# Kernel optimization log

Hardware: AMD Instinct MI355X
Metric: run time of the kernel (lower is better)

Reference implementation:

```python
import jax, jax.numpy as jnp
import numpy as np

N = 30000      # nodes of type 'A'
IN = 128       # in_channels = hidden*2
H = 64         # hidden_channels
OUT = 64
M = 4          # number of metapaths (seq len for attention)
E = 480000     # edges per relation
NH = 8         # num_heads
HD = OUT // NH # head dim = 8
FF = 2048      # transformer dim_feedforward (torch default)
L = 2          # transformer layers
EPS = 1e-5


def setup_inputs() -> dict:
    key = jax.random.key(0)
    ks = iter(jax.random.split(key, 64))
    nk = lambda: next(ks)
    rn = lambda shape, s=0.05: (jax.random.normal(nk(), shape, jnp.float32) * s)
    x = jax.random.normal(nk(), (N, IN), jnp.float32)
    edge_index = jax.random.randint(nk(), (M, 2, E), 0, N, dtype=jnp.int32)
    counts = jnp.array([3.0, 1.0, 2.0, 2.0], jnp.float32)
    mp_weights = counts / counts.sum()
    inp = dict(x=x, edge_index=edge_index, mp_weights=mp_weights,
               W0=rn((M, H, IN)), b0=rn((M, H)), Wl=rn((M, H, IN)), bl=rn((M, H)),
               W1=rn((M, H, IN)), b1=rn((M, H)), Wo=rn((M, OUT, H)), bo=rn((M, OUT)),
               tinw=rn((L, 3 * OUT, OUT)), tinb=rn((L, 3 * OUT)),
               tow=rn((L, OUT, OUT)), tob=rn((L, OUT)),
               ln1g=jnp.ones((L, OUT)), ln1b=jnp.zeros((L, OUT)),
               ff1w=rn((L, FF, OUT)), ff1b=rn((L, FF)),
               ff2w=rn((L, OUT, FF)), ff2b=rn((L, OUT)),
               ln2g=jnp.ones((L, OUT)), ln2b=jnp.zeros((L, OUT)),
               r1w=rn((OUT, OUT)), r1b=rn((OUT,)), r2w=rn((1, OUT)), r2b=rn((1,)))
    return inp


def _layer_norm(v, g, b):
    mu = v.mean(-1, keepdims=True)
    var = ((v - mu) ** 2).mean(-1, keepdims=True)
    return (v - mu) / jnp.sqrt(var + EPS) * g + b


def reference(x, edge_index, mp_weights, W0, b0, Wl, bl, W1, b1, Wo, bo,
              tinw, tinb, tow, tob, ln1g, ln1b, ff1w, ff1b, ff2w, ff2b,
              ln2g, ln2b, r1w, r1b, r2w, r2b):
    n = x.shape[0]
    # ---- per-metapath GNN: gather + scatter-add + 3 fused linears ----
    embs = []
    for m in range(M):
        src, dst = edge_index[m, 0], edge_index[m, 1]
        # flow='target_to_source', aggr='add': agg[i] = sum_{e: src[e]==i} h[dst[e]]
        agg = jnp.zeros_like(x).at[src].add(x[dst])
        # w_l(agg) + w_0(h) + w_1(x), with h == x (forward passes x=h=h_dict[dst])
        h = jax.nn.relu(agg @ Wl[m].T + bl[m] + x @ (W0[m] + W1[m]).T + (b0[m] + b1[m]))
        embs.append(h @ Wo[m].T + bo[m])  # out_proj on updated start-type feats
    e = jnp.stack(embs, axis=1) * mp_weights[None, :, None]  # (N, M, OUT)

    # ---- 2-layer post-norm TransformerEncoder (batch_first, eval/no dropout) ----
    for l in range(L):
        qkv = e @ tinw[l].T + tinb[l]                       # (N, M, 3*OUT)
        q, k, v = jnp.split(qkv, 3, axis=-1)
        split = lambda t: t.reshape(n, M, NH, HD).transpose(0, 2, 1, 3)  # (N,NH,M,HD)
        q, k, v = split(q), split(k), split(v)
        attn = jax.nn.softmax(jnp.einsum('nhqd,nhkd->nhqk', q, k) / np.float32(np.sqrt(HD)), axis=-1)
        o = jnp.einsum('nhqk,nhkd->nhqd', attn, v).transpose(0, 2, 1, 3).reshape(n, M, OUT)
        o = o @ tow[l].T + tob[l]
        e = _layer_norm(e + o, ln1g[l], ln1b[l])
        f = jax.nn.relu(e @ ff1w[l].T + ff1b[l]) @ ff2w[l].T + ff2b[l]
        e = _layer_norm(e + f, ln2g[l], ln2b[l])

    pooled = e.mean(axis=1)                                  # (N, OUT)
    out = jax.nn.relu(pooled @ r1w.T + r1b) @ r2w.T + r2b    # (N, 1)
    return out[:, 0]
```

## Files before the change

kernel.cpp:

```cpp
#include <hip/hip_runtime.h>
#include <hip/hip_bf16.h>
#include <math.h>

#define N_NODES 30000
#define M_P     4
#define E_EDGES 480000
#define N_TOK   (N_NODES * 4)
#define N_ROWS  (M_P * N_NODES)
#define SLOTS   30
#define LN_EPS  1e-5f

typedef short bf16x8 __attribute__((ext_vector_type(8)));
typedef float f32x4  __attribute__((ext_vector_type(4)));
#define MFMA_B16(a, b, c) __builtin_amdgcn_mfma_f32_16x16x32_bf16(a, b, c, 0, 0, 0)

__device__ inline unsigned short f2bf(float f) {
    union { float f; unsigned u; } v; v.f = f;
    unsigned r = v.u + 0x7fffu + ((v.u >> 16) & 1u);
    return (unsigned short)(r >> 16);
}
__device__ inline unsigned pack2bf(float a, float b) {
    union { __hip_bfloat162 h; unsigned u; } cv;
    cv.h = __float22bfloat162_rn(make_float2(a, b));
    return cv.u;
}
__device__ inline float bf2f(short s) {
    union { unsigned u; float f; } v; v.u = ((unsigned)(unsigned short)s) << 16;
    return v.f;
}
__device__ inline bf16x8 mk_frag(const float4& a, const float4& b) {
    union { uint4 u; bf16x8 v; } cv;
    cv.u = make_uint4(pack2bf(a.x, a.y), pack2bf(a.z, a.w),
                      pack2bf(b.x, b.y), pack2bf(b.z, b.w));
    return cv.v;
}

__global__ __launch_bounds__(256) void k_wshuf_gnn(
    const float* __restrict__ Wl, const float* __restrict__ W0, const float* __restrict__ W1,
    unsigned short* __restrict__ wgnn)
{
    const int g = blockIdx.x * 256 + threadIdx.x;
    const int which = g >> 15;
    const int r = g & 32767;
    const int m = r >> 13;
    const int r2 = r & 8191;
    const int row = r2 >> 7, k = r2 & 127;
    const int ot = row >> 4, mm = row & 15;
    const int hh = k >> 5, q = (k >> 3) & 3, j = k & 7;
    float v;
    if (which == 0) v = Wl[(m * 64 + row) * 128 + k];
    else            v = W0[(m * 64 + row) * 128 + k] + W1[(m * 64 + row) * 128 + k];
    wgnn[((which * 4 + m) * 16 + ot * 4 + hh) * 512 + (q * 16 + mm) * 8 + j] = f2bf(v);
}

__global__ __launch_bounds__(256) void k_lin_mfma(
    const float* __restrict__ x, const unsigned short* __restrict__ wgnn,
    const float* __restrict__ b0, const float* __restrict__ bl, const float* __restrict__ b1,
    float* __restrict__ y, float* __restrict__ z)
{
    const int t = threadIdx.x;
    const int w = t >> 6, lane = t & 63;
    const int m_ = lane & 15, qc = lane >> 4;
    const int mw = blockIdx.y;
    const int which = mw >> 2, m = mw & 3;
    const int node = blockIdx.x * 64 + w * 16 + m_;

    bf16x8 xb[4];
    #pragma unroll
    for (int hh = 0; hh < 4; ++hh) {
        float4 a = make_float4(0.f, 0.f, 0.f, 0.f), b = a;
        if (node < N_NODES) {
            a = *(const float4*)(x + node * 128 + hh * 32 + qc * 8);
            b = *(const float4*)(x + node * 128 + hh * 32 + qc * 8 + 4);
        }
        xb[hh] = mk_frag(a, b);
    }

    const unsigned short* Wg = wgnn + mw * 16 * 512;
    f32x4 acc[4];
    #pragma unroll
    for (int ot = 0; ot < 4; ++ot) {
        f32x4 c = {};
        if (which) {
            const int o = m * 64 + ot * 16 + qc * 4;
            const float4 v0 = *(const float4*)(b0 + o);
            const float4 v1 = *(const float4*)(b1 + o);
            const float4 vl = *(const float4*)(bl + o);
            c[0] = v0.x + v1.x + vl.x; c[1] = v0.y + v1.y + vl.y;
            c[2] = v0.z + v1.z + vl.z; c[3] = v0.w + v1.w + vl.w;
        }
        #pragma unroll
        for (int hh = 0; hh < 4; ++hh) {
            const bf16x8 wa = *(const bf16x8*)(Wg + (ot * 4 + hh) * 512 + lane * 8);
            c = MFMA_B16(wa, xb[hh], c);
        }
        acc[ot] = c;
    }
    float* outp = which ? z : y;
    if (node < N_NODES) {
        #pragma unroll
        for (int ot = 0; ot < 4; ++ot)
            *(float4*)(outp + ((size_t)m * N_NODES + node) * 64 + ot * 16 + qc * 4) =
                *(float4*)&acc[ot];
    }
}

__global__ __launch_bounds__(256) void k_fill(
    const int* __restrict__ ei, unsigned short* __restrict__ bins,
    const float* __restrict__ y, float* __restrict__ aggh)
{
    const int base = blockIdx.x * 1024 + threadIdx.x;
    int rows[4], dsts[4];
    #pragma unroll
    for (int i = 0; i < 4; ++i) {
        const int g = base + i * 256;
        const int m = g / E_EDGES;
        const int e = g - m * E_EDGES;
        rows[i] = m * N_NODES + ei[(m * 2) * E_EDGES + e];
        dsts[i] = ei[(m * 2 + 1) * E_EDGES + e];
    }
    int pos[4];
    #pragma unroll
    for (int i = 0; i < 4; ++i)
        pos[i] = atomicAdd((int*)bins + rows[i] * 16, 1);
    #pragma unroll
    for (int i = 0; i < 4; ++i) {
        if (pos[i] < SLOTS) {
            bins[rows[i] * 32 + 2 + pos[i]] = (unsigned short)dsts[i];
        } else {
            const int m = rows[i] / N_NODES;
            const float* yr = y + ((size_t)m * N_NODES + dsts[i]) * 64;
            for (int f = 0; f < 64; ++f)
                unsafeAtomicAdd(&aggh[(size_t)rows[i] * 64 + f], yr[f]);
        }
    }
}

__global__ __launch_bounds__(256) void k_gather(
    const unsigned short* __restrict__ bins,
    const float* __restrict__ y, float* __restrict__ aggh)
{
    const int w = threadIdx.x >> 6, lane = threadIdx.x & 63;
    const int row = blockIdx.x * 4 + w;
    const int m = row / N_NODES;
    const float* ym = y + (size_t)m * N_NODES * 64;
    const int v = (lane < 32) ? bins[row * 32 + lane] : 0;
    const int v0 = __shfl(v, 0), v1 = __shfl(v, 1);
    const int tot = (v0 & 0xffff) | (v1 << 16);
    const int cnt = min(tot, SLOTS);
    float a0 = (tot > SLOTS) ? aggh[(size_t)row * 64 + lane] : 0.f;
    float a1 = 0.f, a2 = 0.f, a3 = 0.f;
    int j = 0;
    for (; j + 4 <= cnt; j += 4) {
        const int r0 = __shfl(v, j + 2), r1 = __shfl(v, j + 3);
        const int r2 = __shfl(v, j + 4), r3 = __shfl(v, j + 5);
        a0 += ym[r0 * 64 + lane]; a1 += ym[r1 * 64 + lane];
        a2 += ym[r2 * 64 + lane]; a3 += ym[r3 * 64 + lane];
    }
    for (; j < cnt; ++j) {
        const int r = __shfl(v, j + 2);
        a0 += ym[r * 64 + lane];
    }
    aggh[(size_t)row * 64 + lane] = (a0 + a1) + (a2 + a3);
}

__global__ __launch_bounds__(256) void k_emb(
    const float* __restrict__ aggh, const float* __restrict__ z,
    const float* __restrict__ Wo, const float* __restrict__ bo,
    const float* __restrict__ mpw, float* __restrict__ e)
{
    __shared__ float hT[64][20];
    __shared__ float WoT[64][64];
    const int t = threadIdx.x;
    const int node0 = blockIdx.x * 16;

    for (int m = 0; m < 4; ++m) {
        #pragma unroll
        for (int i = 0; i < 4; ++i) {
            const int o  = (t & 15) + 16 * i;
            const int kq = t >> 4;
            const float4 v = *(const float4*)(Wo + (m * 64 + o) * 64 + kq * 4);
            WoT[kq * 4 + 0][o] = v.x; WoT[kq * 4 + 1][o] = v.y;
            WoT[kq * 4 + 2][o] = v.z; WoT[kq * 4 + 3][o] = v.w;
        }
        {
            const int node = t & 15, kq = t >> 4;
            const int n = node0 + node;
            const float4 a = *(const float4*)(aggh + (m * N_NODES + n) * 64 + kq * 4);
            const float4 b = *(const float4*)(z + (m * N_NODES + n) * 64 + kq * 4);
            hT[kq * 4 + 0][node] = fmaxf(a.x + b.x, 0.f);
            hT[kq * 4 + 1][node] = fmaxf(a.y + b.y, 0.f);
            hT[kq * 4 + 2][node] = fmaxf(a.z + b.z, 0.f);
            hT[kq * 4 + 3][node] = fmaxf(a.w + b.w, 0.f);
        }
        __syncthreads();
        const int o = t & 63, nl4 = (t >> 6) * 4;
        float acc[4] = {};
        #pragma unroll 8
        for (int k = 0; k < 64; ++k) {
            const float bw = WoT[k][o];
            const float4 a = *(const float4*)&hT[k][nl4];
            acc[0] += a.x * bw; acc[1] += a.y * bw; acc[2] += a.z * bw; acc[3] += a.w * bw;
        }
        const float bb = bo[m * 64 + o];
        const float w  = mpw[m];
        #pragma unroll
        for (int i = 0; i < 4; ++i)
            e[((node0 + nl4 + i) * 4 + m) * 64 + o] = (acc[i] + bb) * w;
        __syncthreads();
    }
}

__global__ __launch_bounds__(256, 3) void k_attn_mfma(
    const float* __restrict__ e,
    const unsigned short* __restrict__ wqkv_s, const float* __restrict__ tinb,
    const unsigned short* __restrict__ tow_s, const float* __restrict__ tob,
    const float* __restrict__ ln1g, const float* __restrict__ ln1b,
    float* __restrict__ eout, int l)
{
    __shared__ __align__(16) short QK[17408];
    __shared__ __align__(16) short Vb[9216];
    const int t = threadIdx.x;
    const int w = t >> 6, lane = t & 63;
    const int m_ = lane & 15, qc = lane >> 4;
    const int tok0 = blockIdx.x * 128;
    short* QKw = &QK[w * 4352];
    short* Vw  = &Vb[w * 2304];

    bf16x8 xb[2][2];
    #pragma unroll
    for (int nt = 0; nt < 2; ++nt)
        #pragma unroll
        for (int h = 0; h < 2; ++h) {
            const int tok = tok0 + w * 32 + nt * 16 + m_;
            const int k0 = h * 32 + qc * 8;
            float4 a = make_float4(0.f, 0.f, 0.f, 0.f), b = a;
            if (tok < N_TOK) {
                a = *(const float4*)(e + tok * 64 + k0);
                b = *(const float4*)(e + tok * 64 + k0 + 4);
            }
            xb[nt][h] = mk_frag(a, b);
        }

    const unsigned short* Wq = wqkv_s + l * 12288;
    f32x4 acc[12][2];
    #pragma unroll
    for (int ft = 0; ft < 12; ++ft) {
        const bf16x8 wa0 = *(const bf16x8*)(Wq + (ft * 2 + 0) * 512 + lane * 8);
        const bf16x8 wa1 = *(const bf16x8*)(Wq + (ft * 2 + 1) * 512 + lane * 8);
        const float4 bv = *(const float4*)(tinb + l * 192 + ft * 16 + qc * 4);
        f32x4 c0; c0[0] = bv.x; c0[1] = bv.y; c0[2] = bv.z; c0[3] = bv.w;
        f32x4 c1 = c0;
        c0 = MFMA_B16(wa0, xb[0][0], c0); c0 = MFMA_B16(wa1, xb[0][1], c0);
        c1 = MFMA_B16(wa0, xb[1][0], c1); c1 = MFMA_B16(wa1, xb[1][1], c1);
        acc[ft][0] = c0; acc[ft][1] = c1;
    }
    #pragma unroll
    for (int ft = 0; ft < 8; ++ft)
        #pragma unroll
        for (int nt = 0; nt < 2; ++nt) {
            const int addr = (nt * 16 + m_) * 136 + ft * 16 + qc * 4;
            *(uint2*)&QKw[addr] = make_uint2(pack2bf(acc[ft][nt][0], acc[ft][nt][1]),
                                             pack2bf(acc[ft][nt][2], acc[ft][nt][3]));
        }
    #pragma unroll
    for (int ft = 8; ft < 12; ++ft)
        #pragma unroll
        for (int nt = 0; nt < 2; ++nt) {
            const int addr = (nt * 16 + m_) * 72 + (ft - 8) * 16 + qc * 4;
            *(uint2*)&Vw[addr] = make_uint2(pack2bf(acc[ft][nt][0], acc[ft][nt][1]),
                                            pack2bf(acc[ft][nt][2], acc[ft][nt][3]));
        }

    {
        const int node = lane >> 3, head = lane & 7;
        float kk[4][8], vv[4][8], qv[4][8];
        #pragma unroll
        for (int j2 = 0; j2 < 4; ++j2) {
            const bf16x8 kr = *(const bf16x8*)&QKw[(node * 4 + j2) * 136 + 64 + head * 8];
            const bf16x8 vr = *(const bf16x8*)&Vw[(node * 4 + j2) * 72 + head * 8];
            const bf16x8 qr = *(const bf16x8*)&QKw[(node * 4 + j2) * 136 + head * 8];
            #pragma unroll
            for (int d = 0; d < 8; ++d) {
                kk[j2][d] = bf2f(kr[d]); vv[j2][d] = bf2f(vr[d]); qv[j2][d] = bf2f(qr[d]);
            }
        }
        const float scale = 0.35355339059327373f;
        const int nt2 = node >> 2, hq = head >> 2, qq = head & 3;
        #pragma unroll
        for (int i = 0; i < 4; ++i) {
            float s[4];
            #pragma unroll
            for (int j2 = 0; j2 < 4; ++j2) {
                float a2 = 0.f;
                #pragma unroll
                for (int d = 0; d < 8; ++d) a2 += qv[i][d] * kk[j2][d];
                s[j2] = a2 * scale;
            }
            const float mx = fmaxf(fmaxf(s[0], s[1]), fmaxf(s[2], s[3]));
            float p[4], sum = 0.f;
            #pragma unroll
            for (int j2 = 0; j2 < 4; ++j2) { p[j2] = __expf(s[j2] - mx); sum += p[j2]; }
            const float inv = 1.f / sum;
            float o[8];
            #pragma unroll
            for (int d = 0; d < 8; ++d)
                o[d] = (p[0] * vv[0][d] + p[1] * vv[1][d] + p[2] * vv[2][d] + p[3] * vv[3][d]) * inv;
            const int n = (node & 3) * 4 + i;
            *(uint4*)&QKw[(nt2 * 2 + hq) * 512 + qq * 128 + n * 8] =
                make_uint4(pack2bf(o[0], o[1]), pack2bf(o[2], o[3]),
                           pack2bf(o[4], o[5]), pack2bf(o[6], o[7]));
        }
    }

    bf16x8 ob[2][2];
    #pragma unroll
    for (int nt = 0; nt < 2; ++nt)
        #pragma unroll
        for (int h = 0; h < 2; ++h)
            ob[nt][h] = *(const bf16x8*)&QKw[(nt * 2 + h) * 512 + lane * 8];
    const unsigned short* Tw = tow_s + l * 4096;
    f32x4 acc2[4][2] = {};
    #pragma unroll
    for (int ot = 0; ot < 4; ++ot) {
        const bf16x8 t0 = *(const bf16x8*)(Tw + (ot * 2 + 0) * 512 + lane * 8);
        const bf16x8 t1 = *(const bf16x8*)(Tw + (ot * 2 + 1) * 512 + lane * 8);
        acc2[ot][0] = MFMA_B16(t0, ob[0][0], acc2[ot][0]);
        acc2[ot][0] = MFMA_B16(t1, ob[0][1], acc2[ot][0]);
        acc2[ot][1] = MFMA_B16(t0, ob[1][0], acc2[ot][1]);
        acc2[ot][1] = MFMA_B16(t1, ob[1][1], acc2[ot][1]);
    }

    float4 tbv[4], gv[4], bv2[4];
    #pragma unroll
    for (int ot = 0; ot < 4; ++ot) {
        const int o = l * 64 + ot * 16 + qc * 4;
        tbv[ot] = *(const float4*)(tob + o);
        gv[ot]  = *(const float4*)(ln1g + o);
        bv2[ot] = *(const float4*)(ln1b + o);
    }
    #pragma unroll
    for (int nt = 0; nt < 2; ++nt) {
        const int tok = tok0 + w * 32 + nt * 16 + m_;
        const bool valid = tok < N_TOK;
        float v[4][4];
        float s = 0.f;
        #pragma unroll
        for (int ot = 0; ot < 4; ++ot) {
            float4 rs = make_float4(0.f, 0.f, 0.f, 0.f);
            if (valid) rs = *(const float4*)(e + tok * 64 + ot * 16 + qc * 4);
            v[ot][0] = acc2[ot][nt][0] + tbv[ot].x + rs.x;
            v[ot][1] = acc2[ot][nt][1] + tbv[ot].y + rs.y;
            v[ot][2] = acc2[ot][nt][2] + tbv[ot].z + rs.z;
            v[ot][3] = acc2[ot][nt][3] + tbv[ot].w + rs.w;
            s += v[ot][0] + v[ot][1] + v[ot][2] + v[ot][3];
        }
        s += __shfl_xor(s, 16); s += __shfl_xor(s, 32);
        const float mean = s * (1.f / 64.f);
        float vs = 0.f;
        #pragma unroll
        for (int ot = 0; ot < 4; ++ot)
            #pragma unroll
            for (int r = 0; r < 4; ++r) { v[ot][r] -= mean; vs += v[ot][r] * v[ot][r]; }
        vs += __shfl_xor(vs, 16); vs += __shfl_xor(vs, 32);
        const float rr = rsqrtf(vs * (1.f / 64.f) + LN_EPS);
        if (valid) {
            #pragma unroll
            for (int ot = 0; ot < 4; ++ot) {
                float4 o4 = make_float4(v[ot][0] * rr * gv[ot].x + bv2[ot].x,
                                        v[ot][1] * rr * gv[ot].y + bv2[ot].y,
                                        v[ot][2] * rr * gv[ot].z + bv2[ot].z,
                                        v[ot][3] * rr * gv[ot].w + bv2[ot].w);
                *(float4*)(eout + tok * 64 + ot * 16 + qc * 4) = o4;
            }
        }
    }
}

__global__ __launch_bounds__(256) void k_wshuf(
    const float* __restrict__ ff1w, const float* __restrict__ ff2w,
    const float* __restrict__ tinw, const float* __restrict__ tow,
    unsigned short* __restrict__ w1s, unsigned short* __restrict__ w2s,
    unsigned short* __restrict__ wqkv_s, unsigned short* __restrict__ tow_s)
{
    const int g = blockIdx.x * 256 + threadIdx.x;
    {
        const int l = g >> 17, r2 = g & 131071;
        const int f = r2 >> 6, k = r2 & 63;
        const int c = f >> 6, fc = f & 63, ft = fc >> 4, m = fc & 15;
        const int h = k >> 5, q = (k >> 3) & 3, j = k & 7;
        w1s[l * 131072 + c * 4096 + (ft * 2 + h) * 512 + (q * 16 + m) * 8 + j] = f2bf(ff1w[g]);
    }
    {
        const int l = g >> 17, r2 = g & 131071;
        const int o = r2 >> 11, f = r2 & 2047;
        const int c = f >> 6, fc = f & 63, h = fc >> 5, q = (fc >> 3) & 3, j = fc & 7;
        const int ot = o >> 4, m = o & 15;
        w2s[l * 131072 + c * 4096 + (ot * 2 + h) * 512 + (q * 16 + m) * 8 + j] = f2bf(ff2w[g]);
    }
    if (g < 2 * 192 * 64) {
        const int l = g / 12288, r2 = g - l * 12288;
        const int f = r2 >> 6, k = r2 & 63;
        const int ft = f >> 4, m = f & 15;
        const int h = k >> 5, q = (k >> 3) & 3, j = k & 7;
        wqkv_s[l * 12288 + (ft * 2 + h) * 512 + (q * 16 + m) * 8 + j] = f2bf(tinw[g]);
    }
    if (g < 2 * 64 * 64) {
        const int l = g >> 12, r2 = g & 4095;
        const int o = r2 >> 6, k = r2 & 63;
        const int ot = o >> 4, m = o & 15;
        const int h = k >> 5, q = (k >> 3) & 3, j = k & 7;
        tow_s[l * 4096 + (ot * 2 + h) * 512 + (q * 16 + m) * 8 + j] = f2bf(tow[g]);
    }
}

__global__ __launch_bounds__(256, 4) void k_ffn_mfma(
    const float* __restrict__ e,
    const unsigned short* __restrict__ w1s, const unsigned short* __restrict__ w2s,
    const float* __restrict__ ff1b, const float* __restrict__ ff2b,
    const float* __restrict__ ln2g, const float* __restrict__ ln2b,
    float* __restrict__ eout, int l)
{
    __shared__ __align__(16) short Act[8192];
    __shared__ __align__(16) short Wb[8192];
    const int t = threadIdx.x;
    const int w = t >> 6, lane = t & 63;
    const int m_ = lane & 15, qc = lane >> 4;
    const int tok0 = blockIdx.x * 128;
    short* Aw = &Act[w * 2048];

    bf16x8 xb[2][2];
    #pragma unroll
    for (int nt = 0; nt < 2; ++nt)
        #pragma unroll
        for (int h = 0; h < 2; ++h) {
            const int tok = tok0 + w * 32 + nt * 16 + m_;
            const int k0 = h * 32 + qc * 8;
            float4 a = make_float4(0.f, 0.f, 0.f, 0.f), b = a;
            if (tok < N_TOK) {
                a = *(const float4*)(e + tok * 64 + k0);
                b = *(const float4*)(e + tok * 64 + k0 + 4);
            }
            xb[nt][h] = mk_frag(a, b);
        }

    const uint4* gw1 = (const uint4*)(w1s + l * 131072);
    const uint4* gw2 = (const uint4*)(w2s + l * 131072);
    uint4 p0 = gw1[t], p1 = gw1[t + 256], p2 = gw2[t], p3 = gw2[t + 256];
    *(uint4*)&Wb[t * 8] = p0;            *(uint4*)&Wb[(t + 256) * 8] = p1;
    *(uint4*)&Wb[4096 + t * 8] = p2;     *(uint4*)&Wb[4096 + (t + 256) * 8] = p3;

    f32x4 acc[4][2] = {};

    for (int c = 0; c < 32; ++c) {
        __syncthreads();
        if (c < 31) {
            p0 = gw1[(c + 1) * 512 + t];       p1 = gw1[(c + 1) * 512 + t + 256];
            p2 = gw2[(c + 1) * 512 + t];       p3 = gw2[(c + 1) * 512 + t + 256];
        }
        #pragma unroll
        for (int ft = 0; ft < 4; ++ft) {
            const bf16x8 wa0 = *(const bf16x8*)&Wb[(ft * 2 + 0) * 512 + lane * 8];
            const bf16x8 wa1 = *(const bf16x8*)&Wb[(ft * 2 + 1) * 512 + lane * 8];
            const float4 bv = *(const float4*)(ff1b + l * 2048 + c * 64 + ft * 16 + qc * 4);
            f32x4 c0; c0[0] = bv.x; c0[1] = bv.y; c0[2] = bv.z; c0[3] = bv.w;
            f32x4 c1 = c0;
            c0 = MFMA_B16(wa0, xb[0][0], c0); c0 = MFMA_B16(wa1, xb[0][1], c0);
            c1 = MFMA_B16(wa0, xb[1][0], c1); c1 = MFMA_B16(wa1, xb[1][1], c1);
            const int ha = ft >> 1, qa = (ft & 1) * 2 + (qc >> 1), jo = (qc & 1) * 4;
            const int boff = ha * 512 + qa * 128 + m_ * 8 + jo;
            *(uint2*)&Aw[boff] =
                make_uint2(pack2bf(fmaxf(c0[0], 0.f), fmaxf(c0[1], 0.f)),
                           pack2bf(fmaxf(c0[2], 0.f), fmaxf(c0[3], 0.f)));
            *(uint2*)&Aw[boff + 1024] =
                make_uint2(pack2bf(fmaxf(c1[0], 0.f), fmaxf(c1[1], 0.f)),
                           pack2bf(fmaxf(c1[2], 0.f), fmaxf(c1[3], 0.f)));
        }
        bf16x8 ab[2][2];
        #pragma unroll
        for (int nt = 0; nt < 2; ++nt)
            #pragma unroll
            for (int h = 0; h < 2; ++h)
                ab[nt][h] = *(const bf16x8*)&Aw[(nt * 2 + h) * 512 + lane * 8];
        #pragma unroll
        for (int ot = 0; ot < 4; ++ot) {
            const bf16x8 w20 = *(const bf16x8*)&Wb[4096 + (ot * 2 + 0) * 512 + lane * 8];
            const bf16x8 w21 = *(const bf16x8*)&Wb[4096 + (ot * 2 + 1) * 512 + lane * 8];
            acc[ot][0] = MFMA_B16(w20, ab[0][0], acc[ot][0]);
            acc[ot][0] = MFMA_B16(w21, ab[0][1], acc[ot][0]);
            acc[ot][1] = MFMA_B16(w20, ab[1][0], acc[ot][1]);
            acc[ot][1] = MFMA_B16(w21, ab[1][1], acc[ot][1]);
        }
        __syncthreads();
        if (c < 31) {
            *(uint4*)&Wb[t * 8] = p0;            *(uint4*)&Wb[(t + 256) * 8] = p1;
            *(uint4*)&Wb[4096 + t * 8] = p2;     *(uint4*)&Wb[4096 + (t + 256) * 8] = p3;
        }
    }

    float4 fb2v[4], gv[4], bv2[4];
    #pragma unroll
    for (int ot = 0; ot < 4; ++ot) {
        const int o = l * 64 + ot * 16 + qc * 4;
        fb2v[ot] = *(const float4*)(ff2b + o);
        gv[ot]   = *(const float4*)(ln2g + o);
        bv2[ot]  = *(const float4*)(ln2b + o);
    }
    #pragma unroll
    for (int nt = 0; nt < 2; ++nt) {
        const int tok = tok0 + w * 32 + nt * 16 + m_;
        const bool valid = tok < N_TOK;
        float v[4][4];
        float s = 0.f;
        #pragma unroll
        for (int ot = 0; ot < 4; ++ot) {
            float4 rs = make_float4(0.f, 0.f, 0.f, 0.f);
            if (valid) rs = *(const float4*)(e + tok * 64 + ot * 16 + qc * 4);
            v[ot][0] = acc[ot][nt][0] + fb2v[ot].x + rs.x;
            v[ot][1] = acc[ot][nt][1] + fb2v[ot].y + rs.y;
            v[ot][2] = acc[ot][nt][2] + fb2v[ot].z + rs.z;
            v[ot][3] = acc[ot][nt][3] + fb2v[ot].w + rs.w;
            s += v[ot][0] + v[ot][1] + v[ot][2] + v[ot][3];
        }
        s += __shfl_xor(s, 16); s += __shfl_xor(s, 32);
        const float mean = s * (1.f / 64.f);
        float vs = 0.f;
        #pragma unroll
        for (int ot = 0; ot < 4; ++ot)
            #pragma unroll
            for (int r = 0; r < 4; ++r) { v[ot][r] -= mean; vs += v[ot][r] * v[ot][r]; }
        vs += __shfl_xor(vs, 16); vs += __shfl_xor(vs, 32);
        const float rr = rsqrtf(vs * (1.f / 64.f) + LN_EPS);
        if (valid) {
            #pragma unroll
            for (int ot = 0; ot < 4; ++ot) {
                float4 o4 = make_float4(v[ot][0] * rr * gv[ot].x + bv2[ot].x,
                                        v[ot][1] * rr * gv[ot].y + bv2[ot].y,
                                        v[ot][2] * rr * gv[ot].z + bv2[ot].z,
                                        v[ot][3] * rr * gv[ot].w + bv2[ot].w);
                *(float4*)(eout + tok * 64 + ot * 16 + qc * 4) = o4;
            }
        }
    }
}

__global__ __launch_bounds__(256) void k_reg(
    const float* __restrict__ e,
    const float* __restrict__ r1w, const float* __restrict__ r1b,
    const float* __restrict__ r2w, const float* __restrict__ r2b,
    float* __restrict__ out)
{
    __shared__ float r1T[64][64];
    __shared__ float pld[4][64];
    const int t = threadIdx.x;
    #pragma unroll
    for (int i = 0; i < 4; ++i) {
        const int j  = (t & 15) + 16 * i;
        const int kq = t >> 4;
        const float4 v = *(const float4*)(r1w + j * 64 + kq * 4);
        r1T[kq * 4 + 0][j] = v.x; r1T[kq * 4 + 1][j] = v.y;
        r1T[kq * 4 + 2][j] = v.z; r1T[kq * 4 + 3][j] = v.w;
    }
    const int w = t >> 6, lane = t & 63;
    const int n = blockIdx.x * 4 + w;
    const float p = 0.25f * (e[(n * 4 + 0) * 64 + lane] + e[(n * 4 + 1) * 64 + lane] +
                             e[(n * 4 + 2) * 64 + lane] + e[(n * 4 + 3) * 64 + lane]);
    pld[w][lane] = p;
    __syncthreads();
    float acc = r1b[lane];
    #pragma unroll 8
    for (int k = 0; k < 64; ++k) acc += pld[w][k] * r1T[k][lane];
    acc = fmaxf(acc, 0.f);
    float partial = acc * r2w[lane];
    partial += __shfl_xor(partial, 1);  partial += __shfl_xor(partial, 2);
    partial += __shfl_xor(partial, 4);  partial += __shfl_xor(partial, 8);
    partial += __shfl_xor(partial, 16); partial += __shfl_xor(partial, 32);
    if (lane == 0) out[n] = partial + r2b[0];
}

extern "C" void kernel_launch(void* const* d_in, const int* in_sizes, int n_in,
                              void* d_out, int out_size, void* d_ws, size_t ws_size,
                              hipStream_t stream) {
    const float* x    = (const float*)d_in[0];
    const int*   ei   = (const int*)d_in[1];
    const float* mpw  = (const float*)d_in[2];
    const float* W0   = (const float*)d_in[3];
    const float* b0   = (const float*)d_in[4];
    const float* Wl   = (const float*)d_in[5];
    const float* bl   = (const float*)d_in[6];
    const float* W1   = (const float*)d_in[7];
    const float* b1   = (const float*)d_in[8];
    const float* Wo   = (const float*)d_in[9];
    const float* bo   = (const float*)d_in[10];
    const float* tinw = (const float*)d_in[11];
    const float* tinb = (const float*)d_in[12];
    const float* tow  = (const float*)d_in[13];
    const float* tob  = (const float*)d_in[14];
    const float* ln1g = (const float*)d_in[15];
    const float* ln1b = (const float*)d_in[16];
    const float* ff1w = (const float*)d_in[17];
    const float* ff1b = (const float*)d_in[18];
    const float* ff2w = (const float*)d_in[19];
    const float* ff2b = (const float*)d_in[20];
    const float* ln2g = (const float*)d_in[21];
    const float* ln2b = (const float*)d_in[22];
    const float* r1w  = (const float*)d_in[23];
    const float* r1b  = (const float*)d_in[24];
    const float* r2w  = (const float*)d_in[25];
    const float* r2b  = (const float*)d_in[26];

    const size_t CH = (size_t)M_P * N_NODES * 64;
    float* y    = (float*)d_ws;
    float* zz   = y + CH;
    float* aggh = zz + CH;
    float* e    = aggh + CH;
    unsigned short* w1s    = (unsigned short*)y;
    unsigned short* w2s    = w1s + 262144;
    unsigned short* wqkv_s = w2s + 262144;
    unsigned short* tow_s  = wqkv_s + 24576;
    unsigned short* bins = (unsigned short*)e;
    unsigned short* wgnn = (unsigned short*)((char*)e + 8 * 1024 * 1024);

    hipMemsetAsync(bins, 0, (size_t)N_ROWS * 64, stream);
    hipMemsetAsync(aggh, 0, CH * sizeof(float), stream);
    k_wshuf_gnn<<<256, 256, 0, stream>>>(Wl, W0, W1, wgnn);
    k_lin_mfma<<<dim3(469, 8), 256, 0, stream>>>(x, wgnn, b0, bl, b1, y, zz);
    k_fill<<<(M_P * E_EDGES) / 1024, 256, 0, stream>>>(ei, bins, y, aggh);
    k_gather<<<N_ROWS / 4, 256, 0, stream>>>(bins, y, aggh);
    k_emb<<<N_NODES / 16, 256, 0, stream>>>(aggh, zz, Wo, bo, mpw, e);
    k_wshuf<<<1024, 256, 0, stream>>>(ff1w, ff2w, tinw, tow, w1s, w2s, wqkv_s, tow_s);
    for (int l = 0; l < 2; ++l) {
        k_attn_mfma<<<(N_TOK + 127) / 128, 256, 0, stream>>>(e, wqkv_s, tinb, tow_s, tob,
                                                             ln1g, ln1b, e, l);
        k_ffn_mfma<<<(N_TOK + 127) / 128, 256, 0, stream>>>(e, w1s, w2s, ff1b, ff2b,
                                                            ln2g, ln2b, e, l);
    }
    k_reg<<<N_NODES / 4, 256, 0, stream>>>(e, r1w, r1b, r2w, r2b, (float*)d_out);
}
```

Before: 596.6 us.

## Fuse edge binning with GNN linear and weight shuffles; add overflow edge list

Edge binning and the per-metapath MFMA linear now run as one launch using disjoint block ranges. This is possible because binning no longer needs y: edges beyond the slot capacity go to a global overflow list instead of doing immediate float atomics into aggh. Each linear block now converts and shuffles its GNN weight tile into LDS itself. The transformer weight shuffle moves into extra blocks of the embedding kernel, and the 30 MB aggh memset is gone. The aim is to cut launches, memsets and serialisation between stages. The cost is redundant per-block weight conversion and a linear scan of the overflow list for every overflowing row, with a fixed capacity that silently drops entries beyond 65536.

```diff
diff --git a/kernel.cpp b/kernel.cpp
--- a/kernel.cpp
+++ b/kernel.cpp
@@ -8,7 +8,11 @@
 #define N_TOK   (N_NODES * 4)
 #define N_ROWS  (M_P * N_NODES)
 #define SLOTS   30
+#define OVF_CAP 65536
 #define LN_EPS  1e-5f
+
+#define NB_FILL 1875
+#define NB_LIN  3752
 
 typedef short bf16x8 __attribute__((ext_vector_type(8)));
 typedef float f32x4  __attribute__((ext_vector_type(4)));
@@ -35,109 +39,109 @@
     return cv.v;
 }
 
-__global__ __launch_bounds__(256) void k_wshuf_gnn(
+__global__ __launch_bounds__(256) void k_phaseA(
+    const int* __restrict__ ei, unsigned short* __restrict__ bins,
+    int* __restrict__ ovf_cnt, int2* __restrict__ ovf,
+    const float* __restrict__ x,
     const float* __restrict__ Wl, const float* __restrict__ W0, const float* __restrict__ W1,
-    unsigned short* __restrict__ wgnn)
-{
-    const int g = blockIdx.x * 256 + threadIdx.x;
-    const int which = g >> 15;
-    const int r = g & 32767;
-    const int m = r >> 13;
-    const int r2 = r & 8191;
-    const int row = r2 >> 7, k = r2 & 127;
-    const int ot = row >> 4, mm = row & 15;
-    const int hh = k >> 5, q = (k >> 3) & 3, j = k & 7;
-    float v;
-    if (which == 0) v = Wl[(m * 64 + row) * 128 + k];
-    else            v = W0[(m * 64 + row) * 128 + k] + W1[(m * 64 + row) * 128 + k];
-    wgnn[((which * 4 + m) * 16 + ot * 4 + hh) * 512 + (q * 16 + mm) * 8 + j] = f2bf(v);
-}
-
-__global__ __launch_bounds__(256) void k_lin_mfma(
-    const float* __restrict__ x, const unsigned short* __restrict__ wgnn,
     const float* __restrict__ b0, const float* __restrict__ bl, const float* __restrict__ b1,
     float* __restrict__ y, float* __restrict__ z)
 {
+    __shared__ __align__(16) short Wf[8192];
+    const int bid = blockIdx.x;
     const int t = threadIdx.x;
-    const int w = t >> 6, lane = t & 63;
-    const int m_ = lane & 15, qc = lane >> 4;
-    const int mw = blockIdx.y;
-    const int which = mw >> 2, m = mw & 3;
-    const int node = blockIdx.x * 64 + w * 16 + m_;
-
-    bf16x8 xb[4];
-    #pragma unroll
-    for (int hh = 0; hh < 4; ++hh) {
-        float4 a = make_float4(0.f, 0.f, 0.f, 0.f), b = a;
+
+    if (bid < NB_FILL) {
+        const int base = bid * 1024 + t;
+        int rows[4], dsts[4];
+        #pragma unroll
+        for (int i = 0; i < 4; ++i) {
+            const int g = base + i * 256;
+            const int m = g / E_EDGES;
+            const int e = g - m * E_EDGES;
+            rows[i] = m * N_NODES + ei[(m * 2) * E_EDGES + e];
+            dsts[i] = ei[(m * 2 + 1) * E_EDGES + e];
+        }
+        int pos[4];
+        #pragma unroll
+        for (int i = 0; i < 4; ++i)
+            pos[i] = atomicAdd((int*)bins + rows[i] * 16, 1);
+        #pragma unroll
+        for (int i = 0; i < 4; ++i) {
+            if (pos[i] < SLOTS) {
+                bins[rows[i] * 32 + 2 + pos[i]] = (unsigned short)dsts[i];
+            } else {
+                const int ix = atomicAdd(ovf_cnt, 1);
+                if (ix < OVF_CAP) ovf[ix] = make_int2(rows[i], dsts[i]);
+            }
+        }
+    } else {
+        const int lid = bid - NB_FILL;
+        const int bx = lid % 469;
+        const int by = lid / 469;
+        const int which = by >> 2, m = by & 3;
+        const int w = t >> 6, lane = t & 63;
+        const int m_ = lane & 15, qc = lane >> 4;
+        const int node = bx * 64 + w * 16 + m_;
+
+        #pragma unroll
+        for (int i = 0; i < 32; ++i) {
+            const int d = t + 256 * i;
+            const int fg = d >> 9, rem = d & 511;
+            const int qmm = rem >> 3, j = d & 7;
+            const int q = qmm >> 4, mm = qmm & 15;
+            const int ot = fg >> 2, hh = fg & 3;
+            const int row = ot * 16 + mm, k = hh * 32 + q * 8 + j;
+            float v;
+            if (which == 0) v = Wl[(m * 64 + row) * 128 + k];
+            else            v = W0[(m * 64 + row) * 128 + k] + W1[(m * 64 + row) * 128 + k];
+            Wf[d] = (short)f2bf(v);
+        }
+
+        bf16x8 xb[4];
+        #pragma unroll
+        for (int hh = 0; hh < 4; ++hh) {
+            float4 a = make_float4(0.f, 0.f, 0.f, 0.f), b = a;
+            if (node < N_NODES) {
+                a = *(const float4*)(x + node * 128 + hh * 32 + qc * 8);
+                b = *(const float4*)(x + node * 128 + hh * 32 + qc * 8 + 4);
+            }
+            xb[hh] = mk_frag(a, b);
+        }
+        __syncthreads();
+
+        f32x4 acc[4];
+        #pragma unroll
+        for (int ot = 0; ot < 4; ++ot) {
+            f32x4 c = {};
+            if (which) {
+                const int o = m * 64 + ot * 16 + qc * 4;
+                const float4 v0 = *(const float4*)(b0 + o);
+                const float4 v1 = *(const float4*)(b1 + o);
+                const float4 vl = *(const float4*)(bl + o);
+                c[0] = v0.x + v1.x + vl.x; c[1] = v0.y + v1.y + vl.y;
+                c[2] = v0.z + v1.z + vl.z; c[3] = v0.w + v1.w + vl.w;
+            }
+            #pragma unroll
+            for (int hh = 0; hh < 4; ++hh) {
+                const bf16x8 wa = *(const bf16x8*)&Wf[(ot * 4 + hh) * 512 + lane * 8];
+                c = MFMA_B16(wa, xb[hh], c);
+            }
+            acc[ot] = c;
+        }
+        float* outp = which ? z : y;
         if (node < N_NODES) {
-            a = *(const float4*)(x + node * 128 + hh * 32 + qc * 8);
-            b = *(const float4*)(x + node * 128 + hh * 32 + qc * 8 + 4);
-        }
-        xb[hh] = mk_frag(a, b);
-    }
-
-    const unsigned short* Wg = wgnn + mw * 16 * 512;
-    f32x4 acc[4];
-    #pragma unroll
-    for (int ot = 0; ot < 4; ++ot) {
-        f32x4 c = {};
-        if (which) {
-            const int o = m * 64 + ot * 16 + qc * 4;
-            const float4 v0 = *(const float4*)(b0 + o);
-            const float4 v1 = *(const float4*)(b1 + o);
-            const float4 vl = *(const float4*)(bl + o);
-            c[0] = v0.x + v1.x + vl.x; c[1] = v0.y + v1.y + vl.y;
-            c[2] = v0.z + v1.z + vl.z; c[3] = v0.w + v1.w + vl.w;
-        }
-        #pragma unroll
-        for (int hh = 0; hh < 4; ++hh) {
-            const bf16x8 wa = *(const bf16x8*)(Wg + (ot * 4 + hh) * 512 + lane * 8);
-            c = MFMA_B16(wa, xb[hh], c);
-        }
-        acc[ot] = c;
-    }
-    float* outp = which ? z : y;
-    if (node < N_NODES) {
-        #pragma unroll
-        for (int ot = 0; ot < 4; ++ot)
-            *(float4*)(outp + ((size_t)m * N_NODES + node) * 64 + ot * 16 + qc * 4) =
-                *(float4*)&acc[ot];
-    }
-}
-
-__global__ __launch_bounds__(256) void k_fill(
-    const int* __restrict__ ei, unsigned short* __restrict__ bins,
-    const float* __restrict__ y, float* __restrict__ aggh)
-{
-    const int base = blockIdx.x * 1024 + threadIdx.x;
-    int rows[4], dsts[4];
-    #pragma unroll
-    for (int i = 0; i < 4; ++i) {
-        const int g = base + i * 256;
-        const int m = g / E_EDGES;
-        const int e = g - m * E_EDGES;
-        rows[i] = m * N_NODES + ei[(m * 2) * E_EDGES + e];
-        dsts[i] = ei[(m * 2 + 1) * E_EDGES + e];
-    }
-    int pos[4];
-    #pragma unroll
-    for (int i = 0; i < 4; ++i)
-        pos[i] = atomicAdd((int*)bins + rows[i] * 16, 1);
-    #pragma unroll
-    for (int i = 0; i < 4; ++i) {
-        if (pos[i] < SLOTS) {
-            bins[rows[i] * 32 + 2 + pos[i]] = (unsigned short)dsts[i];
-        } else {
-            const int m = rows[i] / N_NODES;
-            const float* yr = y + ((size_t)m * N_NODES + dsts[i]) * 64;
-            for (int f = 0; f < 64; ++f)
-                unsafeAtomicAdd(&aggh[(size_t)rows[i] * 64 + f], yr[f]);
+            #pragma unroll
+            for (int ot = 0; ot < 4; ++ot)
+                *(float4*)(outp + ((size_t)m * N_NODES + node) * 64 + ot * 16 + qc * 4) =
+                    *(float4*)&acc[ot];
         }
     }
 }
 
 __global__ __launch_bounds__(256) void k_gather(
     const unsigned short* __restrict__ bins,
+    const int* __restrict__ ovf_cnt, const int2* __restrict__ ovf,
     const float* __restrict__ y, float* __restrict__ aggh)
 {
     const int w = threadIdx.x >> 6, lane = threadIdx.x & 63;
@@ -148,8 +152,7 @@
     const int v0 = __shfl(v, 0), v1 = __shfl(v, 1);
     const int tot = (v0 & 0xffff) | (v1 << 16);
     const int cnt = min(tot, SLOTS);
-    float a0 = (tot > SLOTS) ? aggh[(size_t)row * 64 + lane] : 0.f;
-    float a1 = 0.f, a2 = 0.f, a3 = 0.f;
+    float a0 = 0.f, a1 = 0.f, a2 = 0.f, a3 = 0.f;
     int j = 0;
     for (; j + 4 <= cnt; j += 4) {
         const int r0 = __shfl(v, j + 2), r1 = __shfl(v, j + 3);
@@ -161,19 +164,64 @@
         const int r = __shfl(v, j + 2);
         a0 += ym[r * 64 + lane];
     }
+    if (tot > SLOTS) {
+        const int no = min(*ovf_cnt, OVF_CAP);
+        for (int i2 = 0; i2 < no; ++i2) {
+            const int2 ent = ovf[i2];
+            if (ent.x == row) a0 += ym[ent.y * 64 + lane];
+        }
+    }
     aggh[(size_t)row * 64 + lane] = (a0 + a1) + (a2 + a3);
 }
 
-__global__ __launch_bounds__(256) void k_emb(
+__global__ __launch_bounds__(256) void k_emb_ws(
     const float* __restrict__ aggh, const float* __restrict__ z,
     const float* __restrict__ Wo, const float* __restrict__ bo,
-    const float* __restrict__ mpw, float* __restrict__ e)
+    const float* __restrict__ mpw, float* __restrict__ e,
+    const float* __restrict__ ff1w, const float* __restrict__ ff2w,
+    const float* __restrict__ tinw, const float* __restrict__ tow,
+    unsigned short* __restrict__ w1s, unsigned short* __restrict__ w2s,
+    unsigned short* __restrict__ wqkv_s, unsigned short* __restrict__ tow_s)
 {
     __shared__ float hT[64][20];
     __shared__ float WoT[64][64];
     const int t = threadIdx.x;
-    const int node0 = blockIdx.x * 16;
-
+    const int bid = blockIdx.x;
+
+    if (bid >= N_NODES / 16) {
+        const int g = (bid - N_NODES / 16) * 256 + t;
+        {
+            const int l = g >> 17, r2 = g & 131071;
+            const int f = r2 >> 6, k = r2 & 63;
+            const int c = f >> 6, fc = f & 63, ft = fc >> 4, m = fc & 15;
+            const int h = k >> 5, q = (k >> 3) & 3, j = k & 7;
+            w1s[l * 131072 + c * 4096 + (ft * 2 + h) * 512 + (q * 16 + m) * 8 + j] = f2bf(ff1w[g]);
+        }
+        {
+            const int l = g >> 17, r2 = g & 131071;
+            const int o = r2 >> 11, f = r2 & 2047;
+            const int c = f >> 6, fc = f & 63, h = fc >> 5, q = (fc >> 3) & 3, j = fc & 7;
+            const int ot = o >> 4, m = o & 15;
+            w2s[l * 131072 + c * 4096 + (ot * 2 + h) * 512 + (q * 16 + m) * 8 + j] = f2bf(ff2w[g]);
+        }
+        if (g < 2 * 192 * 64) {
+            const int l = g / 12288, r2 = g - l * 12288;
+            const int f = r2 >> 6, k = r2 & 63;
+            const int ft = f >> 4, m = f & 15;
+            const int h = k >> 5, q = (k >> 3) & 3, j = k & 7;
+            wqkv_s[l * 12288 + (ft * 2 + h) * 512 + (q * 16 + m) * 8 + j] = f2bf(tinw[g]);
+        }
+        if (g < 2 * 64 * 64) {
+            const int l = g >> 12, r2 = g & 4095;
+            const int o = r2 >> 6, k = r2 & 63;
+            const int ot = o >> 4, m = o & 15;
+            const int h = k >> 5, q = (k >> 3) & 3, j = k & 7;
+            tow_s[l * 4096 + (ot * 2 + h) * 512 + (q * 16 + m) * 8 + j] = f2bf(tow[g]);
+        }
+        return;
+    }
+
+    const int node0 = bid * 16;
     for (int m = 0; m < 4; ++m) {
         #pragma unroll
         for (int i = 0; i < 4; ++i) {
@@ -374,43 +422,6 @@
                 *(float4*)(eout + tok * 64 + ot * 16 + qc * 4) = o4;
             }
         }
-    }
-}
-
-__global__ __launch_bounds__(256) void k_wshuf(
-    const float* __restrict__ ff1w, const float* __restrict__ ff2w,
-    const float* __restrict__ tinw, const float* __restrict__ tow,
-    unsigned short* __restrict__ w1s, unsigned short* __restrict__ w2s,
-    unsigned short* __restrict__ wqkv_s, unsigned short* __restrict__ tow_s)
-{
-    const int g = blockIdx.x * 256 + threadIdx.x;
-    {
-        const int l = g >> 17, r2 = g & 131071;
-        const int f = r2 >> 6, k = r2 & 63;
-        const int c = f >> 6, fc = f & 63, ft = fc >> 4, m = fc & 15;
-        const int h = k >> 5, q = (k >> 3) & 3, j = k & 7;
-        w1s[l * 131072 + c * 4096 + (ft * 2 + h) * 512 + (q * 16 + m) * 8 + j] = f2bf(ff1w[g]);
-    }
-    {
-        const int l = g >> 17, r2 = g & 131071;
-        const int o = r2 >> 11, f = r2 & 2047;
-        const int c = f >> 6, fc = f & 63, h = fc >> 5, q = (fc >> 3) & 3, j = fc & 7;
-        const int ot = o >> 4, m = o & 15;
-        w2s[l * 131072 + c * 4096 + (ot * 2 + h) * 512 + (q * 16 + m) * 8 + j] = f2bf(ff2w[g]);
-    }
-    if (g < 2 * 192 * 64) {
-        const int l = g / 12288, r2 = g - l * 12288;
-        const int f = r2 >> 6, k = r2 & 63;
-        const int ft = f >> 4, m = f & 15;
-        const int h = k >> 5, q = (k >> 3) & 3, j = k & 7;
-        wqkv_s[l * 12288 + (ft * 2 + h) * 512 + (q * 16 + m) * 8 + j] = f2bf(tinw[g]);
-    }
-    if (g < 2 * 64 * 64) {
-        const int l = g >> 12, r2 = g & 4095;
-        const int o = r2 >> 6, k = r2 & 63;
-        const int ot = o >> 4, m = o & 15;
-        const int h = k >> 5, q = (k >> 3) & 3, j = k & 7;
-        tow_s[l * 4096 + (ot * 2 + h) * 512 + (q * 16 + m) * 8 + j] = f2bf(tow[g]);
     }
 }
 
@@ -619,16 +630,16 @@
     unsigned short* wqkv_s = w2s + 262144;
     unsigned short* tow_s  = wqkv_s + 24576;
     unsigned short* bins = (unsigned short*)e;
-    unsigned short* wgnn = (unsigned short*)((char*)e + 8 * 1024 * 1024);
-
-    hipMemsetAsync(bins, 0, (size_t)N_ROWS * 64, stream);
-    hipMemsetAsync(aggh, 0, CH * sizeof(float), stream);
-    k_wshuf_gnn<<<256, 256, 0, stream>>>(Wl, W0, W1, wgnn);
-    k_lin_mfma<<<dim3(469, 8), 256, 0, stream>>>(x, wgnn, b0, bl, b1, y, zz);
-    k_fill<<<(M_P * E_EDGES) / 1024, 256, 0, stream>>>(ei, bins, y, aggh);
-    k_gather<<<N_ROWS / 4, 256, 0, stream>>>(bins, y, aggh);
-    k_emb<<<N_NODES / 16, 256, 0, stream>>>(aggh, zz, Wo, bo, mpw, e);
-    k_wshuf<<<1024, 256, 0, stream>>>(ff1w, ff2w, tinw, tow, w1s, w2s, wqkv_s, tow_s);
+    int* ovf_cnt = (int*)((char*)e + (size_t)N_ROWS * 64);
+    int2* ovf    = (int2*)((char*)ovf_cnt + 16);
+
+    hipMemsetAsync(bins, 0, (size_t)N_ROWS * 64 + 16, stream);
+    k_phaseA<<<NB_FILL + NB_LIN, 256, 0, stream>>>(ei, bins, ovf_cnt, ovf,
+                                                   x, Wl, W0, W1, b0, bl, b1, y, zz);
+    k_gather<<<N_ROWS / 4, 256, 0, stream>>>(bins, ovf_cnt, ovf, y, aggh);
+    k_emb_ws<<<N_NODES / 16 + 1024, 256, 0, stream>>>(aggh, zz, Wo, bo, mpw, e,
+                                                      ff1w, ff2w, tinw, tow,
+                                                      w1s, w2s, wqkv_s, tow_s);
     for (int l = 0; l < 2; ++l) {
         k_attn_mfma<<<(N_TOK + 127) / 128, 256, 0, stream>>>(e, wqkv_s, tinb, tow_s, tob,
                                                              ln1g, ln1b, e, l);
```

New measurement: 582.4 us. 1.02x faster.
